# Optimization experiments

Measured on AMD Instinct MI355X. Metric: run time of the kernel, lower is better.

## Reference

```python
import jax, jax.numpy as jnp
import numpy as np

CHUNK_SIZE = 1024  # module default chunk_size


def setup_inputs() -> dict:
    key = jax.random.key(0)
    kq, kk, kv = jax.random.split(key, 3)
    B, H, S, D = 2, 16, 2048, 64
    q = jax.random.normal(kq, (B, H, S, D), dtype=jnp.float32)
    k = jax.random.normal(kk, (B, H, S, D), dtype=jnp.float32)
    v = jax.random.normal(kv, (B, H, S, D), dtype=jnp.float32)
    return {"q": q, "k": k, "v": v}


def reference(q, k, v):
    # Chunked causal attention: q split into chunks of CHUNK_SIZE along seq,
    # each chunk attends to the full K/V with causal mask (tril, diagonal=start).
    B, H, S, D = q.shape
    scale = D ** (-0.5)
    cs = CHUNK_SIZE
    nc = S // cs  # S is a multiple of chunk_size here
    qc = q.reshape(B, H, nc, cs, D)
    # scores: [B, H, nc, cs, S]
    scores = jnp.einsum('bhncd,bhsd->bhncs', qc, k) * scale
    # causal mask per chunk: key position j visible iff j <= chunk_start + i
    row = (jnp.arange(nc) * cs)[:, None, None] + jnp.arange(cs)[None, :, None]  # [nc, cs, 1]
    col = jnp.arange(S)[None, None, :]  # [1, 1, S]
    causal = col <= row  # [nc, cs, S]
    scores = jnp.where(causal[None, None], scores, -jnp.inf)
    attn = jax.nn.softmax(scores, axis=-1)
    out = jnp.einsum('bhncs,bhsd->bhncd', attn, v)
    return out.reshape(B, H, S, D)
```

## Files before the change

### kernel.cpp

```cpp
#include <hip/hip_runtime.h>

typedef __bf16 bf16x8 __attribute__((ext_vector_type(8)));
typedef float f32x4 __attribute__((ext_vector_type(4)));

#define S_LEN 2048
#define D_DIM 64

__global__ __launch_bounds__(256, 4) void attn_fwd(const float* __restrict__ Q,
                                                   const float* __restrict__ K,
                                                   const float* __restrict__ V,
                                                   float* __restrict__ O) {
    const int b    = blockIdx.x;
    const int xcd  = b & 7;
    const int cs   = (b >> 3) & 31;
    const int j    = b >> 8;
    const int head = xcd * 4 + (cs >> 3);
    const int slot = cs & 7;
    const int chunk = (j == 0) ? slot : (j == 1) ? (31 - slot)
                    : (j == 2) ? (slot + 8) : (23 - slot);

    const int tid  = threadIdx.x;
    const int wave = tid >> 6;
    const int lane = tid & 63;
    const int l15  = lane & 15;
    const int lhi  = lane >> 4;

    const int q0 = chunk * 64 + wave * 16;
    const size_t base = (size_t)head * (S_LEN * D_DIM);
    const float qscale = 0.125f * 1.44269504088896340736f;

    __shared__ __align__(16) __bf16 Klds[2][64][64];
    __shared__ __align__(16) __bf16 Vt[2][64][64];
    __shared__ __align__(16) __bf16 Plds[4][16][64];

    const int rk = tid >> 2;
    const int ck = (tid & 3) << 4;
    const int kp = tid & 31;
    const int dc = tid >> 5;
    const int swk = (rk & 7) << 3;

    bf16x8 qf[2];
    {
        const float* qrow = Q + base + (size_t)(q0 + l15) * D_DIM + lhi * 8;
        #pragma unroll
        for (int h = 0; h < 2; ++h) {
            f32x4 a = *(const f32x4*)(qrow + h * 32);
            f32x4 bq = *(const f32x4*)(qrow + h * 32 + 4);
            bf16x8 t;
            #pragma unroll
            for (int e = 0; e < 4; ++e) { t[e] = (__bf16)(a[e] * qscale); t[e + 4] = (__bf16)(bq[e] * qscale); }
            qf[h] = t;
        }
    }

    f32x4 acc[4];
    #pragma unroll
    for (int td = 0; td < 4; ++td) acc[td] = (f32x4){0.f, 0.f, 0.f, 0.f};
    float m_r = -1e30f, l_r = 0.f;

    f32x4 pk[4], pva[2], pvb[2];

    {
        const float* ks = K + base + (size_t)rk * D_DIM + ck;
        #pragma unroll
        for (int i = 0; i < 4; ++i) pk[i] = *(const f32x4*)(ks + 4 * i);
        const float* v0 = V + base + (size_t)(2 * kp) * D_DIM + dc * 8;
        pva[0] = *(const f32x4*)v0;           pva[1] = *(const f32x4*)(v0 + 4);
        pvb[0] = *(const f32x4*)(v0 + D_DIM); pvb[1] = *(const f32x4*)(v0 + D_DIM + 4);
        bf16x8 k0, k1;
        #pragma unroll
        for (int e = 0; e < 4; ++e) {
            k0[e] = (__bf16)pk[0][e]; k0[e + 4] = (__bf16)pk[1][e];
            k1[e] = (__bf16)pk[2][e]; k1[e + 4] = (__bf16)pk[3][e];
        }
        *(bf16x8*)&Klds[0][rk][ck ^ swk] = k0;
        *(bf16x8*)&Klds[0][rk][(ck + 8) ^ swk] = k1;
        #pragma unroll
        for (int jj = 0; jj < 8; ++jj) {
            const int d = dc * 8 + jj;
            const float av = (jj < 4) ? pva[0][jj & 3] : pva[1][jj & 3];
            const float bv = (jj < 4) ? pvb[0][jj & 3] : pvb[1][jj & 3];
            union { __bf16 h[2]; unsigned int u; } t;
            t.h[0] = (__bf16)av; t.h[1] = (__bf16)bv;
            *(unsigned int*)&Vt[0][d][(2 * kp) ^ ((d & 7) << 3)] = t.u;
        }
    }

    const int nt = chunk + 1;
    for (int kt = 0; kt < nt; ++kt) {
        const int cur = kt & 1;
        __syncthreads();

        const bool pre = (kt + 1 < nt);
        if (pre) {
            const int kv1 = (kt + 1) << 6;
            const float* ks = K + base + (size_t)(kv1 + rk) * D_DIM + ck;
            #pragma unroll
            for (int i = 0; i < 4; ++i) pk[i] = *(const f32x4*)(ks + 4 * i);
            const float* v0 = V + base + (size_t)(kv1 + 2 * kp) * D_DIM + dc * 8;
            pva[0] = *(const f32x4*)v0;           pva[1] = *(const f32x4*)(v0 + 4);
            pvb[0] = *(const f32x4*)(v0 + D_DIM); pvb[1] = *(const f32x4*)(v0 + D_DIM + 4);
        }

        f32x4 s[4];
        #pragma unroll
        for (int ct = 0; ct < 4; ++ct) s[ct] = (f32x4){0.f, 0.f, 0.f, 0.f};
        __builtin_amdgcn_s_setprio(1);
        #pragma unroll
        for (int h = 0; h < 2; ++h) {
            #pragma unroll
            for (int ct = 0; ct < 4; ++ct) {
                const int krow = ct * 16 + l15;
                bf16x8 kf = *(const bf16x8*)&Klds[cur][krow][(h * 32 + lhi * 8) ^ ((l15 & 7) << 3)];
                s[ct] = __builtin_amdgcn_mfma_f32_16x16x32_bf16(kf, qf[h], s[ct], 0, 0, 0);
            }
        }
        __builtin_amdgcn_s_setprio(0);

        if (kt == nt - 1) {
            const int kv0 = kt << 6;
            const int qg = q0 + l15;
            #pragma unroll
            for (int ct = 0; ct < 4; ++ct)
                #pragma unroll
                for (int r = 0; r < 4; ++r) {
                    const int kg = kv0 + ct * 16 + lhi * 4 + r;
                    if (kg > qg) s[ct][r] = -1e30f;
                }
        }

        float mm = fmaxf(fmaxf(fmaxf(s[0][0], s[0][1]), fmaxf(s[0][2], s[0][3])),
                         fmaxf(fmaxf(s[1][0], s[1][1]), fmaxf(s[1][2], s[1][3])));
        mm = fmaxf(mm, fmaxf(fmaxf(fmaxf(s[2][0], s[2][1]), fmaxf(s[2][2], s[2][3])),
                             fmaxf(fmaxf(s[3][0], s[3][1]), fmaxf(s[3][2], s[3][3]))));
        mm = fmaxf(mm, __shfl_xor(mm, 16));
        mm = fmaxf(mm, __shfl_xor(mm, 32));
        if (!__all(mm - m_r <= 8.0f)) {
            const float mn = fmaxf(m_r, mm);
            const float f = exp2f(m_r - mn);
            m_r = mn;
            l_r *= f;
            #pragma unroll
            for (int r = 0; r < 4; ++r) {
                const float fr = __shfl(f, lhi * 4 + r);
                #pragma unroll
                for (int td = 0; td < 4; ++td) acc[td][r] *= fr;
            }
        }
        float ps = 0.f;
        #pragma unroll
        for (int ct = 0; ct < 4; ++ct)
            #pragma unroll
            for (int r = 0; r < 4; ++r) {
                const float p = exp2f(s[ct][r] - m_r);
                s[ct][r] = p;
                ps += p;
            }
        ps += __shfl_xor(ps, 16);
        ps += __shfl_xor(ps, 32);
        l_r += ps;

        #pragma unroll
        for (int ct = 0; ct < 4; ++ct) {
            union { __bf16 h[4]; unsigned long long u; } pw;
            #pragma unroll
            for (int r = 0; r < 4; ++r) pw.h[r] = (__bf16)s[ct][r];
            *(unsigned long long*)&Plds[wave][l15][(ct * 16 + lhi * 4) ^ ((l15 & 7) << 3)] = pw.u;
        }
        asm volatile("s_waitcnt lgkmcnt(0)" ::: "memory");
        bf16x8 pf[2];
        #pragma unroll
        for (int kh = 0; kh < 2; ++kh)
            pf[kh] = *(const bf16x8*)&Plds[wave][l15][(kh * 32 + lhi * 8) ^ ((l15 & 7) << 3)];
        asm volatile("" ::: "memory");

        __builtin_amdgcn_s_setprio(1);
        #pragma unroll
        for (int kh = 0; kh < 2; ++kh) {
            #pragma unroll
            for (int td = 0; td < 4; ++td) {
                const int vrow = td * 16 + l15;
                bf16x8 vf = *(const bf16x8*)&Vt[cur][vrow][(kh * 32 + lhi * 8) ^ ((vrow & 7) << 3)];
                acc[td] = __builtin_amdgcn_mfma_f32_16x16x32_bf16(pf[kh], vf, acc[td], 0, 0, 0);
            }
        }
        __builtin_amdgcn_s_setprio(0);

        if (pre) {
            const int nxt = cur ^ 1;
            bf16x8 k0, k1;
            #pragma unroll
            for (int e = 0; e < 4; ++e) {
                k0[e] = (__bf16)pk[0][e]; k0[e + 4] = (__bf16)pk[1][e];
                k1[e] = (__bf16)pk[2][e]; k1[e + 4] = (__bf16)pk[3][e];
            }
            *(bf16x8*)&Klds[nxt][rk][ck ^ swk] = k0;
            *(bf16x8*)&Klds[nxt][rk][(ck + 8) ^ swk] = k1;
            #pragma unroll
            for (int jj = 0; jj < 8; ++jj) {
                const int d = dc * 8 + jj;
                const float av = (jj < 4) ? pva[0][jj & 3] : pva[1][jj & 3];
                const float bv = (jj < 4) ? pvb[0][jj & 3] : pvb[1][jj & 3];
                union { __bf16 h[2]; unsigned int u; } t;
                t.h[0] = (__bf16)av; t.h[1] = (__bf16)bv;
                *(unsigned int*)&Vt[nxt][d][(2 * kp) ^ ((d & 7) << 3)] = t.u;
            }
        }
    }

    float* orow = O + base + (size_t)q0 * D_DIM;
    #pragma unroll
    for (int r = 0; r < 4; ++r) {
        const float inv = 1.0f / __shfl(l_r, lhi * 4 + r);
        #pragma unroll
        for (int td = 0; td < 4; ++td)
            orow[(size_t)(lhi * 4 + r) * D_DIM + td * 16 + l15] = acc[td][r] * inv;
    }
}

extern "C" void kernel_launch(void* const* d_in, const int* in_sizes, int n_in,
                              void* d_out, int out_size, void* d_ws, size_t ws_size,
                              hipStream_t stream) {
    const float* q = (const float*)d_in[0];
    const float* k = (const float*)d_in[1];
    const float* v = (const float*)d_in[2];
    float* o = (float*)d_out;
    attn_fwd<<<dim3(1024), dim3(256), 0, stream>>>(q, k, v, o);
}
```

Baseline: 58.46 us.

## Rewrite attention with 32x32 MFMA, paired causal chunks, and register-resident P

The kernel moves from 16x16x32 to 32x32x16 bf16 MFMA, with each wave owning 32 query rows. Each block now handles two complementary 128-row query chunks (cA and 15-cA) in one fixed 34-tile loop, which balances causal work across 512 blocks. The P matrix is handed to the PV MFMA through v_cvt_pk_bf16_f32 and v_permlane32_swap instead of an LDS round trip. The cost is much higher register pressure (launch bounds drop to 2) and fewer blocks.

After: 84.92 us. 45.3% more time.

```diff
diff --git a/kernel.cpp b/kernel.cpp
--- a/kernel.cpp
+++ b/kernel.cpp
@@ -2,36 +2,38 @@
 
 typedef __bf16 bf16x8 __attribute__((ext_vector_type(8)));
 typedef float f32x4 __attribute__((ext_vector_type(4)));
+typedef float f32x16 __attribute__((ext_vector_type(16)));
 
 #define S_LEN 2048
 #define D_DIM 64
 
-__global__ __launch_bounds__(256, 4) void attn_fwd(const float* __restrict__ Q,
-                                                   const float* __restrict__ K,
-                                                   const float* __restrict__ V,
-                                                   float* __restrict__ O) {
+__global__ __launch_bounds__(256, 2) void attn32p(const float* __restrict__ Q,
+                                                  const float* __restrict__ K,
+                                                  const float* __restrict__ V,
+                                                  float* __restrict__ O) {
     const int b    = blockIdx.x;
     const int xcd  = b & 7;
-    const int cs   = (b >> 3) & 31;
+    const int cu   = (b >> 3) & 31;
     const int j    = b >> 8;
-    const int head = xcd * 4 + (cs >> 3);
-    const int slot = cs & 7;
-    const int chunk = (j == 0) ? slot : (j == 1) ? (31 - slot)
-                    : (j == 2) ? (slot + 8) : (23 - slot);
+    const int head = xcd * 4 + (cu >> 3);
+    const int pr   = (cu & 7) + (j << 3);
+    const int cA   = pr;
+    const int cB   = 15 - pr;
+    const int nA   = 2 * cA + 2;
+    const int NT   = 34;
 
     const int tid  = threadIdx.x;
     const int wave = tid >> 6;
     const int lane = tid & 63;
-    const int l15  = lane & 15;
-    const int lhi  = lane >> 4;
-
-    const int q0 = chunk * 64 + wave * 16;
+    const int l31  = lane & 31;
+    const int hi   = lane >> 5;
+    const int sw31 = (l31 & 7) << 3;
+
     const size_t base = (size_t)head * (S_LEN * D_DIM);
     const float qscale = 0.125f * 1.44269504088896340736f;
 
     __shared__ __align__(16) __bf16 Klds[2][64][64];
     __shared__ __align__(16) __bf16 Vt[2][64][64];
-    __shared__ __align__(16) __bf16 Plds[4][16][64];
 
     const int rk = tid >> 2;
     const int ck = (tid & 3) << 4;
@@ -39,42 +41,48 @@
     const int dc = tid >> 5;
     const int swk = (rk & 7) << 3;
 
-    bf16x8 qf[2];
+    bf16x8 qcur[4], qfB[4];
     {
-        const float* qrow = Q + base + (size_t)(q0 + l15) * D_DIM + lhi * 8;
-        #pragma unroll
-        for (int h = 0; h < 2; ++h) {
-            f32x4 a = *(const f32x4*)(qrow + h * 32);
-            f32x4 bq = *(const f32x4*)(qrow + h * 32 + 4);
-            bf16x8 t;
-            #pragma unroll
-            for (int e = 0; e < 4; ++e) { t[e] = (__bf16)(a[e] * qscale); t[e + 4] = (__bf16)(bq[e] * qscale); }
-            qf[h] = t;
+        const float* qa = Q + base + (size_t)(cA * 128 + wave * 32 + l31) * D_DIM + hi * 8;
+        const float* qb = Q + base + (size_t)(cB * 128 + wave * 32 + l31) * D_DIM + hi * 8;
+        #pragma unroll
+        for (int kd = 0; kd < 4; ++kd) {
+            f32x4 a0 = *(const f32x4*)(qa + kd * 16), a1 = *(const f32x4*)(qa + kd * 16 + 4);
+            f32x4 b0 = *(const f32x4*)(qb + kd * 16), b1 = *(const f32x4*)(qb + kd * 16 + 4);
+            bf16x8 ta, tb;
+            #pragma unroll
+            for (int e = 0; e < 4; ++e) {
+                ta[e] = (__bf16)(a0[e] * qscale); ta[e + 4] = (__bf16)(a1[e] * qscale);
+                tb[e] = (__bf16)(b0[e] * qscale); tb[e + 4] = (__bf16)(b1[e] * qscale);
+            }
+            qcur[kd] = ta; qfB[kd] = tb;
         }
     }
 
-    f32x4 acc[4];
+    f32x16 acc0, acc1;
     #pragma unroll
-    for (int td = 0; td < 4; ++td) acc[td] = (f32x4){0.f, 0.f, 0.f, 0.f};
+    for (int r = 0; r < 16; ++r) { acc0[r] = 0.f; acc1[r] = 0.f; }
     float m_r = -1e30f, l_r = 0.f;
+    int q0w = cA * 128 + wave * 32;
 
     f32x4 pk[4], pva[2], pvb[2];
-
-    {
-        const float* ks = K + base + (size_t)rk * D_DIM + ck;
+    auto loadRegs = [&](int kv0) {
+        const float* ks = K + base + (size_t)(kv0 + rk) * D_DIM + ck;
         #pragma unroll
         for (int i = 0; i < 4; ++i) pk[i] = *(const f32x4*)(ks + 4 * i);
-        const float* v0 = V + base + (size_t)(2 * kp) * D_DIM + dc * 8;
+        const float* v0 = V + base + (size_t)(kv0 + 2 * kp) * D_DIM + dc * 8;
         pva[0] = *(const f32x4*)v0;           pva[1] = *(const f32x4*)(v0 + 4);
         pvb[0] = *(const f32x4*)(v0 + D_DIM); pvb[1] = *(const f32x4*)(v0 + D_DIM + 4);
+    };
+    auto writeRegs = [&](int bufi) {
         bf16x8 k0, k1;
         #pragma unroll
         for (int e = 0; e < 4; ++e) {
             k0[e] = (__bf16)pk[0][e]; k0[e + 4] = (__bf16)pk[1][e];
             k1[e] = (__bf16)pk[2][e]; k1[e + 4] = (__bf16)pk[3][e];
         }
-        *(bf16x8*)&Klds[0][rk][ck ^ swk] = k0;
-        *(bf16x8*)&Klds[0][rk][(ck + 8) ^ swk] = k1;
+        *(bf16x8*)&Klds[bufi][rk][ck ^ swk] = k0;
+        *(bf16x8*)&Klds[bufi][rk][(ck + 8) ^ swk] = k1;
         #pragma unroll
         for (int jj = 0; jj < 8; ++jj) {
             const int d = dc * 8 + jj;
@@ -82,139 +90,155 @@
             const float bv = (jj < 4) ? pvb[0][jj & 3] : pvb[1][jj & 3];
             union { __bf16 h[2]; unsigned int u; } t;
             t.h[0] = (__bf16)av; t.h[1] = (__bf16)bv;
-            *(unsigned int*)&Vt[0][d][(2 * kp) ^ ((d & 7) << 3)] = t.u;
+            *(unsigned int*)&Vt[bufi][d][(2 * kp) ^ ((d & 7) << 3)] = t.u;
+        }
+    };
+    auto cvtpk = [](float lo, float hh) {
+        unsigned int r;
+        asm("v_cvt_pk_bf16_f32 %0, %1, %2" : "=v"(r) : "v"(lo), "v"(hh));
+        return r;
+    };
+
+    loadRegs(0);
+    writeRegs(0);
+
+    for (int t = 0; t < NT; ++t) {
+        const int cur = t & 1;
+        __syncthreads();
+
+        if (t + 1 < NT)
+            loadRegs((t + 1 < nA) ? ((t + 1) << 6) : ((t + 1 - nA) << 6));
+        const int kv0 = (t < nA) ? (t << 6) : ((t - nA) << 6);
+
+        if (kv0 <= q0w + 31) {
+            f32x16 s0, s1;
+            #pragma unroll
+            for (int r = 0; r < 16; ++r) { s0[r] = 0.f; s1[r] = 0.f; }
+            __builtin_amdgcn_s_setprio(1);
+            #pragma unroll
+            for (int kd = 0; kd < 4; ++kd) {
+                bf16x8 kf0 = *(const bf16x8*)&Klds[cur][l31][(kd * 16 + hi * 8) ^ sw31];
+                bf16x8 kf1 = *(const bf16x8*)&Klds[cur][32 + l31][(kd * 16 + hi * 8) ^ sw31];
+                s0 = __builtin_amdgcn_mfma_f32_32x32x16_bf16(kf0, qcur[kd], s0, 0, 0, 0);
+                s1 = __builtin_amdgcn_mfma_f32_32x32x16_bf16(kf1, qcur[kd], s1, 0, 0, 0);
+            }
+            __builtin_amdgcn_s_setprio(0);
+
+            if (kv0 + 63 > q0w) {
+                const int qg = q0w + l31;
+                #pragma unroll
+                for (int r = 0; r < 16; ++r) {
+                    const int cr = (r & 3) + 8 * (r >> 2) + 4 * hi;
+                    if (kv0 + cr > qg)      s0[r] = -1e30f;
+                    if (kv0 + 32 + cr > qg) s1[r] = -1e30f;
+                }
+            }
+
+            float tr[16];
+            #pragma unroll
+            for (int r = 0; r < 16; ++r) tr[r] = fmaxf(s0[r], s1[r]);
+            #pragma unroll
+            for (int off = 8; off >= 1; off >>= 1)
+                #pragma unroll
+                for (int r = 0; r < 16; ++r) if (r < off) tr[r] = fmaxf(tr[r], tr[r + off]);
+            float mm = fmaxf(tr[0], __shfl_xor(tr[0], 32));
+            if (!__all(mm - m_r <= 8.0f)) {
+                const float mn = fmaxf(m_r, mm);
+                const float f = exp2f(m_r - mn);
+                m_r = mn;
+                l_r *= f;
+                #pragma unroll
+                for (int r = 0; r < 16; ++r) {
+                    const float fr = __shfl(f, (r & 3) + 8 * (r >> 2) + 4 * hi);
+                    acc0[r] *= fr; acc1[r] *= fr;
+                }
+            }
+            float u[16];
+            #pragma unroll
+            for (int r = 0; r < 16; ++r) {
+                s0[r] = exp2f(s0[r] - m_r);
+                s1[r] = exp2f(s1[r] - m_r);
+                u[r] = s0[r] + s1[r];
+            }
+            #pragma unroll
+            for (int off = 8; off >= 1; off >>= 1)
+                #pragma unroll
+                for (int r = 0; r < 16; ++r) if (r < off) u[r] += u[r + off];
+            l_r += u[0] + __shfl_xor(u[0], 32);
+
+            __builtin_amdgcn_s_setprio(1);
+            {
+                unsigned int w01 = cvtpk(s0[0],  s0[1]),  w23 = cvtpk(s0[2],  s0[3]);
+                unsigned int w45 = cvtpk(s0[4],  s0[5]),  w67 = cvtpk(s0[6],  s0[7]);
+                unsigned int w89 = cvtpk(s0[8],  s0[9]),  wab = cvtpk(s0[10], s0[11]);
+                unsigned int wcd = cvtpk(s0[12], s0[13]), wef = cvtpk(s0[14], s0[15]);
+                asm("v_permlane32_swap_b32 %0, %1" : "+v"(w01), "+v"(w45));
+                asm("v_permlane32_swap_b32 %0, %1" : "+v"(w23), "+v"(w67));
+                asm("v_permlane32_swap_b32 %0, %1" : "+v"(w89), "+v"(wcd));
+                asm("v_permlane32_swap_b32 %0, %1" : "+v"(wab), "+v"(wef));
+                union { unsigned int u[4]; bf16x8 v; } f0 = {{w01, w23, w45, w67}};
+                union { unsigned int u[4]; bf16x8 v; } f1 = {{w89, wab, wcd, wef}};
+                bf16x8 v00 = *(const bf16x8*)&Vt[cur][l31][(hi * 8) ^ sw31];
+                bf16x8 v01 = *(const bf16x8*)&Vt[cur][32 + l31][(hi * 8) ^ sw31];
+                acc0 = __builtin_amdgcn_mfma_f32_32x32x16_bf16(f0.v, v00, acc0, 0, 0, 0);
+                acc1 = __builtin_amdgcn_mfma_f32_32x32x16_bf16(f0.v, v01, acc1, 0, 0, 0);
+                bf16x8 v10 = *(const bf16x8*)&Vt[cur][l31][(16 + hi * 8) ^ sw31];
+                bf16x8 v11 = *(const bf16x8*)&Vt[cur][32 + l31][(16 + hi * 8) ^ sw31];
+                acc0 = __builtin_amdgcn_mfma_f32_32x32x16_bf16(f1.v, v10, acc0, 0, 0, 0);
+                acc1 = __builtin_amdgcn_mfma_f32_32x32x16_bf16(f1.v, v11, acc1, 0, 0, 0);
+            }
+            {
+                unsigned int w01 = cvtpk(s1[0],  s1[1]),  w23 = cvtpk(s1[2],  s1[3]);
+                unsigned int w45 = cvtpk(s1[4],  s1[5]),  w67 = cvtpk(s1[6],  s1[7]);
+                unsigned int w89 = cvtpk(s1[8],  s1[9]),  wab = cvtpk(s1[10], s1[11]);
+                unsigned int wcd = cvtpk(s1[12], s1[13]), wef = cvtpk(s1[14], s1[15]);
+                asm("v_permlane32_swap_b32 %0, %1" : "+v"(w01), "+v"(w45));
+                asm("v_permlane32_swap_b32 %0, %1" : "+v"(w23), "+v"(w67));
+                asm("v_permlane32_swap_b32 %0, %1" : "+v"(w89), "+v"(wcd));
+                asm("v_permlane32_swap_b32 %0, %1" : "+v"(wab), "+v"(wef));
+                union { unsigned int u[4]; bf16x8 v; } f2 = {{w01, w23, w45, w67}};
+                union { unsigned int u[4]; bf16x8 v; } f3 = {{w89, wab, wcd, wef}};
+                bf16x8 v20 = *(const bf16x8*)&Vt[cur][l31][(32 + hi * 8) ^ sw31];
+                bf16x8 v21 = *(const bf16x8*)&Vt[cur][32 + l31][(32 + hi * 8) ^ sw31];
+                acc0 = __builtin_amdgcn_mfma_f32_32x32x16_bf16(f2.v, v20, acc0, 0, 0, 0);
+                acc1 = __builtin_amdgcn_mfma_f32_32x32x16_bf16(f2.v, v21, acc1, 0, 0, 0);
+                bf16x8 v30 = *(const bf16x8*)&Vt[cur][l31][(48 + hi * 8) ^ sw31];
+                bf16x8 v31 = *(const bf16x8*)&Vt[cur][32 + l31][(48 + hi * 8) ^ sw31];
+                acc0 = __builtin_amdgcn_mfma_f32_32x32x16_bf16(f3.v, v30, acc0, 0, 0, 0);
+                acc1 = __builtin_amdgcn_mfma_f32_32x32x16_bf16(f3.v, v31, acc1, 0, 0, 0);
+            }
+            __builtin_amdgcn_s_setprio(0);
+        }
+
+        if (t + 1 < NT) writeRegs(cur ^ 1);
+
+        if (t == nA - 1) {
+            const float inv_own = 1.0f / l_r;
+            float* ob = O + base + (size_t)(cA * 128 + wave * 32) * D_DIM + l31;
+            #pragma unroll
+            for (int r = 0; r < 16; ++r) {
+                const int cr = (r & 3) + 8 * (r >> 2) + 4 * hi;
+                const float inv = __shfl(inv_own, cr);
+                ob[(size_t)cr * D_DIM]      = acc0[r] * inv;
+                ob[(size_t)cr * D_DIM + 32] = acc1[r] * inv;
+            }
+            #pragma unroll
+            for (int r = 0; r < 16; ++r) { acc0[r] = 0.f; acc1[r] = 0.f; }
+            m_r = -1e30f; l_r = 0.f;
+            #pragma unroll
+            for (int kd = 0; kd < 4; ++kd) qcur[kd] = qfB[kd];
+            q0w = cB * 128 + wave * 32;
         }
     }
 
-    const int nt = chunk + 1;
-    for (int kt = 0; kt < nt; ++kt) {
-        const int cur = kt & 1;
-        __syncthreads();
-
-        const bool pre = (kt + 1 < nt);
-        if (pre) {
-            const int kv1 = (kt + 1) << 6;
-            const float* ks = K + base + (size_t)(kv1 + rk) * D_DIM + ck;
-            #pragma unroll
-            for (int i = 0; i < 4; ++i) pk[i] = *(const f32x4*)(ks + 4 * i);
-            const float* v0 = V + base + (size_t)(kv1 + 2 * kp) * D_DIM + dc * 8;
-            pva[0] = *(const f32x4*)v0;           pva[1] = *(const f32x4*)(v0 + 4);
-            pvb[0] = *(const f32x4*)(v0 + D_DIM); pvb[1] = *(const f32x4*)(v0 + D_DIM + 4);
-        }
-
-        f32x4 s[4];
-        #pragma unroll
-        for (int ct = 0; ct < 4; ++ct) s[ct] = (f32x4){0.f, 0.f, 0.f, 0.f};
-        __builtin_amdgcn_s_setprio(1);
-        #pragma unroll
-        for (int h = 0; h < 2; ++h) {
-            #pragma unroll
-            for (int ct = 0; ct < 4; ++ct) {
-                const int krow = ct * 16 + l15;
-                bf16x8 kf = *(const bf16x8*)&Klds[cur][krow][(h * 32 + lhi * 8) ^ ((l15 & 7) << 3)];
-                s[ct] = __builtin_amdgcn_mfma_f32_16x16x32_bf16(kf, qf[h], s[ct], 0, 0, 0);
-            }
-        }
-        __builtin_amdgcn_s_setprio(0);
-
-        if (kt == nt - 1) {
-            const int kv0 = kt << 6;
-            const int qg = q0 + l15;
-            #pragma unroll
-            for (int ct = 0; ct < 4; ++ct)
-                #pragma unroll
-                for (int r = 0; r < 4; ++r) {
-                    const int kg = kv0 + ct * 16 + lhi * 4 + r;
-                    if (kg > qg) s[ct][r] = -1e30f;
-                }
-        }
-
-        float mm = fmaxf(fmaxf(fmaxf(s[0][0], s[0][1]), fmaxf(s[0][2], s[0][3])),
-                         fmaxf(fmaxf(s[1][0], s[1][1]), fmaxf(s[1][2], s[1][3])));
-        mm = fmaxf(mm, fmaxf(fmaxf(fmaxf(s[2][0], s[2][1]), fmaxf(s[2][2], s[2][3])),
-                             fmaxf(fmaxf(s[3][0], s[3][1]), fmaxf(s[3][2], s[3][3]))));
-        mm = fmaxf(mm, __shfl_xor(mm, 16));
-        mm = fmaxf(mm, __shfl_xor(mm, 32));
-        if (!__all(mm - m_r <= 8.0f)) {
-            const float mn = fmaxf(m_r, mm);
-            const float f = exp2f(m_r - mn);
-            m_r = mn;
-            l_r *= f;
-            #pragma unroll
-            for (int r = 0; r < 4; ++r) {
-                const float fr = __shfl(f, lhi * 4 + r);
-                #pragma unroll
-                for (int td = 0; td < 4; ++td) acc[td][r] *= fr;
-            }
-        }
-        float ps = 0.f;
-        #pragma unroll
-        for (int ct = 0; ct < 4; ++ct)
-            #pragma unroll
-            for (int r = 0; r < 4; ++r) {
-                const float p = exp2f(s[ct][r] - m_r);
-                s[ct][r] = p;
-                ps += p;
-            }
-        ps += __shfl_xor(ps, 16);
-        ps += __shfl_xor(ps, 32);
-        l_r += ps;
-
-        #pragma unroll
-        for (int ct = 0; ct < 4; ++ct) {
-            union { __bf16 h[4]; unsigned long long u; } pw;
-            #pragma unroll
-            for (int r = 0; r < 4; ++r) pw.h[r] = (__bf16)s[ct][r];
-            *(unsigned long long*)&Plds[wave][l15][(ct * 16 + lhi * 4) ^ ((l15 & 7) << 3)] = pw.u;
-        }
-        asm volatile("s_waitcnt lgkmcnt(0)" ::: "memory");
-        bf16x8 pf[2];
-        #pragma unroll
-        for (int kh = 0; kh < 2; ++kh)
-            pf[kh] = *(const bf16x8*)&Plds[wave][l15][(kh * 32 + lhi * 8) ^ ((l15 & 7) << 3)];
-        asm volatile("" ::: "memory");
-
-        __builtin_amdgcn_s_setprio(1);
-        #pragma unroll
-        for (int kh = 0; kh < 2; ++kh) {
-            #pragma unroll
-            for (int td = 0; td < 4; ++td) {
-                const int vrow = td * 16 + l15;
-                bf16x8 vf = *(const bf16x8*)&Vt[cur][vrow][(kh * 32 + lhi * 8) ^ ((vrow & 7) << 3)];
-                acc[td] = __builtin_amdgcn_mfma_f32_16x16x32_bf16(pf[kh], vf, acc[td], 0, 0, 0);
-            }
-        }
-        __builtin_amdgcn_s_setprio(0);
-
-        if (pre) {
-            const int nxt = cur ^ 1;
-            bf16x8 k0, k1;
-            #pragma unroll
-            for (int e = 0; e < 4; ++e) {
-                k0[e] = (__bf16)pk[0][e]; k0[e + 4] = (__bf16)pk[1][e];
-                k1[e] = (__bf16)pk[2][e]; k1[e + 4] = (__bf16)pk[3][e];
-            }
-            *(bf16x8*)&Klds[nxt][rk][ck ^ swk] = k0;
-            *(bf16x8*)&Klds[nxt][rk][(ck + 8) ^ swk] = k1;
-            #pragma unroll
-            for (int jj = 0; jj < 8; ++jj) {
-                const int d = dc * 8 + jj;
-                const float av = (jj < 4) ? pva[0][jj & 3] : pva[1][jj & 3];
-                const float bv = (jj < 4) ? pvb[0][jj & 3] : pvb[1][jj & 3];
-                union { __bf16 h[2]; unsigned int u; } t;
-                t.h[0] = (__bf16)av; t.h[1] = (__bf16)bv;
-                *(unsigned int*)&Vt[nxt][d][(2 * kp) ^ ((d & 7) << 3)] = t.u;
-            }
-        }
-    }
-
-    float* orow = O + base + (size_t)q0 * D_DIM;
+    const float inv_own = 1.0f / l_r;
+    float* ob = O + base + (size_t)(cB * 128 + wave * 32) * D_DIM + l31;
     #pragma unroll
-    for (int r = 0; r < 4; ++r) {
-        const float inv = 1.0f / __shfl(l_r, lhi * 4 + r);
-        #pragma unroll
-        for (int td = 0; td < 4; ++td)
-            orow[(size_t)(lhi * 4 + r) * D_DIM + td * 16 + l15] = acc[td][r] * inv;
+    for (int r = 0; r < 16; ++r) {
+        const int cr = (r & 3) + 8 * (r >> 2) + 4 * hi;
+        const float inv = __shfl(inv_own, cr);
+        ob[(size_t)cr * D_DIM]      = acc0[r] * inv;
+        ob[(size_t)cr * D_DIM + 32] = acc1[r] * inv;
     }
 }
 
@@ -225,5 +249,5 @@
     const float* k = (const float*)d_in[1];
     const float* v = (const float*)d_in[2];
     float* o = (float*)d_out;
-    attn_fwd<<<dim3(1024), dim3(256), 0, stream>>>(q, k, v, o);
+    attn32p<<<dim3(512), dim3(256), 0, stream>>>(q, k, v, o);
 }
```
